# Performance work log

Measured on AMD Instinct MI355X. Metric: run time of the kernel, lower is better.

The kernel has to match this reference:

```python
import jax, jax.numpy as jnp
import numpy as np

SCALING_FACTOR = 1.0


def setup_inputs() -> dict:
    key = jax.random.key(0)
    k1, k2, k3 = jax.random.split(key, 3)
    B, N1, N2, DX, DZ, NT, NK = 4, 64, 64, 2, 128, 2048, 2
    x_grid = jax.random.uniform(k1, (B, N1, N2, DX), dtype=jnp.float32)
    z_grid = jax.random.normal(k2, (B, N1, N2, DZ), dtype=jnp.float32)
    xt = jax.random.uniform(k3, (B, NT, DX), dtype=jnp.float32)
    # Replicates torch init: logspace around log10(init_lengthscale), inverse-softplus
    init_ls = np.logspace(np.log10(0.1) - 0.5, np.log10(0.1) + 0.5, NK).astype(np.float32)
    init_ls = np.tile(init_ls[None, :], (DX, 1))  # (dim, num_kernels)
    lengthscale_param = jnp.asarray(np.log(np.expm1(init_ls)))
    return {"x_grid": x_grid, "z_grid": z_grid, "xt": xt, "lengthscale_param": lengthscale_param}


def reference(x_grid, z_grid, xt, lengthscale_param):
    B = x_grid.shape[0]
    xg = x_grid.reshape(B, -1, x_grid.shape[-1])   # (b, ng, dx)
    zg = z_grid.reshape(B, -1, z_grid.shape[-1])   # (b, ng, dz)
    ls = 1e-5 + jax.nn.softplus(lengthscale_param)  # (dx, nk)
    # EQ/RBF weights: (b, nt, ng, nk)
    diff = (xt[:, :, None, :, None] - xg[:, None, :, :, None]) / ls[None, None, None]
    weights = jnp.exp(-0.5 * jnp.sum(diff * diff, axis=3))
    # weighted smoothing: per-kernel matmul weights @ z_grid, then interleave as (dz nk)
    out = jnp.einsum('btgk,bgz->btzk', weights, zg) / SCALING_FACTOR  # (b, nt, dz, nk)
    return out.reshape(B, xt.shape[1], -1)  # (b, nt, dz*nk), nk fastest like 'b nt (dz nk)'
```

## Files before the change

### kernel.cpp

```cpp
#include <hip/hip_runtime.h>
#include <hip/hip_bf16.h>
#include <cmath>

#define B_   4
#define NT_  2048
#define G_   4096
#define DZ_  128

typedef __attribute__((ext_vector_type(8))) short bf16x8;
typedef __attribute__((ext_vector_type(8))) short s16x8;
typedef __attribute__((ext_vector_type(4))) float f32x4;

__device__ __forceinline__ float softplus_f(float x) {
    return fmaxf(x, 0.0f) + log1pf(expf(-fabsf(x)));
}

__device__ __forceinline__ void gl2lds16(const void* gsrc, void* ldst) {
    __builtin_amdgcn_global_load_lds(
        (const __attribute__((address_space(1))) unsigned int*)gsrc,
        (__attribute__((address_space(3))) unsigned int*)ldst, 16, 0, 0);
}

__global__ __launch_bounds__(256, 1)
void transpose_z(const float* __restrict__ z, unsigned short* __restrict__ zt)
{
    __shared__ unsigned short tile[64][66];
    const int bx = blockIdx.x;
    const int zti = bx & 1;
    const int gt  = (bx >> 1) & 63;
    const int b   = bx >> 7;
    const int g0 = gt * 64, z0 = zti * 64;
    const int tid = threadIdx.x;
    const int zl = tid & 63, gl = tid >> 6;
    #pragma unroll
    for (int i = 0; i < 16; ++i) {
        const int g = gl + i * 4;
        const float v = z[(size_t)(b * G_ + g0 + g) * DZ_ + z0 + zl];
        unsigned int u = __float_as_uint(v);
        u = u + 0x7FFFu + ((u >> 16) & 1u);
        tile[g][zl] = (unsigned short)(u >> 16);
    }
    __syncthreads();
    const int nt  = tid >> 6;
    const int q   = (tid >> 4) & 3;
    const int fl  = tid & 15;
    #pragma unroll
    for (int i = 0; i < 2; ++i) {
        s16x8 v;
        #pragma unroll
        for (int j = 0; j < 8; ++j)
            v[j] = (short)tile[i * 32 + q * 8 + j][nt * 16 + fl];
        *(s16x8*)(zt + ((size_t)(b * 128 + gt * 2 + i) * 8 + zti * 4 + nt) * 512
                  + (size_t)(q * 16 + fl) * 8) = v;
    }
}

__global__ __launch_bounds__(512, 4)
void setconv_main(const float* __restrict__ xt,
                  const float* __restrict__ xg,
                  const float* __restrict__ lsp,
                  const unsigned short* __restrict__ Zt,
                  float* __restrict__ out)
{
    __shared__ __align__(16) unsigned short lds[32768];

    const int bx = blockIdx.x;
    const int b  = (bx >> 1) & 3;
    const int tt = ((bx >> 3) << 1) | (bx & 1);
    const int tid  = threadIdx.x;
    const int w    = tid >> 6;
    const int lane = tid & 63;
    const int quad = lane >> 4;
    const int l15  = lane & 15;
    const int t0   = tt * 16;

    float c00, c01, c10, c11;
    {
        const float h = -0.72134752f;
        float ls;
        ls = 1e-5f + softplus_f(lsp[0]); c00 = h / (ls * ls);
        ls = 1e-5f + softplus_f(lsp[1]); c01 = h / (ls * ls);
        ls = 1e-5f + softplus_f(lsp[2]); c10 = h / (ls * ls);
        ls = 1e-5f + softplus_f(lsp[3]); c11 = h / (ls * ls);
    }

    const float xt0 = xt[(size_t)(b * NT_ + t0 + l15) * 2 + 0];
    const float xt1 = xt[(size_t)(b * NT_ + t0 + l15) * 2 + 1];

    f32x4 acc[2][8];
    #pragma unroll
    for (int k = 0; k < 2; ++k)
        #pragma unroll
        for (int n = 0; n < 8; ++n) acc[k][n] = (f32x4)0.0f;

    unsigned short* const mytile = lds + w * 4096;
    const float* xgq = xg + (size_t)(b * G_ + w * 512 + quad * 8) * 2;

    float4 xv0 = *(const float4*)(xgq + 0);
    float4 xv1 = *(const float4*)(xgq + 4);
    float4 xv2 = *(const float4*)(xgq + 8);
    float4 xv3 = *(const float4*)(xgq + 12);
    {
        const unsigned short* zs = Zt + (size_t)(b * 128 + w * 16) * 4096 + lane * 8;
        #pragma unroll
        for (int i = 0; i < 8; ++i)
            gl2lds16(zs + i * 512, mytile + i * 512);
    }

    #pragma unroll
    for (int ch = 0; ch < 16; ++ch) {
        float gx[8], gy[8];
        gx[0]=xv0.x; gy[0]=xv0.y; gx[1]=xv0.z; gy[1]=xv0.w;
        gx[2]=xv1.x; gy[2]=xv1.y; gx[3]=xv1.z; gy[3]=xv1.w;
        gx[4]=xv2.x; gy[4]=xv2.y; gx[5]=xv2.z; gy[5]=xv2.w;
        gx[6]=xv3.x; gy[6]=xv3.y; gx[7]=xv3.z; gy[7]=xv3.w;
        unsigned int w0b[8], w1b[8];
        #pragma unroll
        for (int j = 0; j < 8; ++j) {
            const float d0 = xt0 - gx[j];
            const float d1 = xt1 - gy[j];
            const float q0 = d0 * d0;
            const float q1 = d1 * d1;
            const float e0 = fmaf(q1, c10, q0 * c00);
            const float e1 = fmaf(q1, c11, q0 * c01);
            w0b[j] = __float_as_uint(__builtin_amdgcn_exp2f(e0));
            w1b[j] = __float_as_uint(__builtin_amdgcn_exp2f(e1));
        }
        union { bf16x8 v; unsigned int u[4]; } a0, a1;
        #pragma unroll
        for (int h = 0; h < 4; ++h) {
            a0.u[h] = __builtin_amdgcn_perm(w0b[2*h+1], w0b[2*h], 0x07060302u);
            a1.u[h] = __builtin_amdgcn_perm(w1b[2*h+1], w1b[2*h], 0x07060302u);
        }

        __builtin_amdgcn_s_waitcnt(0x0F70);
        if (ch < 15) {
            const float* xp = xgq + (ch + 1) * 64;
            xv0 = *(const float4*)(xp + 0);
            xv1 = *(const float4*)(xp + 4);
            xv2 = *(const float4*)(xp + 8);
            xv3 = *(const float4*)(xp + 12);
        }

        #pragma unroll
        for (int nt = 0; nt < 8; ++nt) {
            const bf16x8 bz = *(const bf16x8*)(mytile + nt * 512 + lane * 8);
            acc[0][nt] = __builtin_amdgcn_mfma_f32_16x16x32_bf16(a0.v, bz, acc[0][nt], 0, 0, 0);
            acc[1][nt] = __builtin_amdgcn_mfma_f32_16x16x32_bf16(a1.v, bz, acc[1][nt], 0, 0, 0);
        }

        if (ch < 15) {
            const unsigned short* zs = Zt + (size_t)(b * 128 + w * 16 + ch + 1) * 4096
                                       + lane * 8;
            #pragma unroll
            for (int i = 0; i < 8; ++i)
                gl2lds16(zs + i * 512, mytile + i * 512);
        }
    }

    float* const red = (float*)lds;
    #define RED_W(slot) { \
        float* bp = &red[(slot) * 4096 + lane * 4]; \
        _Pragma("unroll") \
        for (int k = 0; k < 2; ++k) \
            _Pragma("unroll") \
            for (int n = 0; n < 8; ++n) \
                *(f32x4*)(bp + (k * 8 + n) * 256) = acc[k][n]; }
    #define RED_A(slot) { \
        const float* bp = &red[(slot) * 4096 + lane * 4]; \
        _Pragma("unroll") \
        for (int k = 0; k < 2; ++k) \
            _Pragma("unroll") \
            for (int n = 0; n < 8; ++n) \
                acc[k][n] += *(const f32x4*)(bp + (k * 8 + n) * 256); }

    __syncthreads();
    if (w >= 4) RED_W(w - 4);
    __syncthreads();
    if (w < 4) RED_A(w);
    if (w == 2 || w == 3) RED_W(w);
    __syncthreads();
    if (w < 2) RED_A(w + 2);
    if (w == 1) RED_W(3);
    __syncthreads();
    if (w == 0) {
        RED_A(3);
        const int tr = t0 + quad * 4;
        #pragma unroll
        for (int nt = 0; nt < 8; ++nt) {
            float* ob = out + (size_t)(b * NT_ + tr) * (DZ_ * 2) + (nt * 16 + l15) * 2;
            #pragma unroll
            for (int r = 0; r < 4; ++r)
                *(float2*)(ob + (size_t)r * (DZ_ * 2)) =
                    make_float2(acc[0][nt][r], acc[1][nt][r]);
        }
    }
    #undef RED_W
    #undef RED_A
}

extern "C" void kernel_launch(void* const* d_in, const int* in_sizes, int n_in,
                              void* d_out, int out_size, void* d_ws, size_t ws_size,
                              hipStream_t stream)
{
    const float* x_grid = (const float*)d_in[0];
    const float* z_grid = (const float*)d_in[1];
    const float* xt     = (const float*)d_in[2];
    const float* lsp    = (const float*)d_in[3];
    float* out = (float*)d_out;
    unsigned short* Zt = (unsigned short*)d_ws;

    hipLaunchKernelGGL(transpose_z, dim3(512), dim3(256), 0, stream, z_grid, Zt);
    hipLaunchKernelGGL(setconv_main, dim3(512), dim3(512), 0, stream,
                       xt, x_grid, lsp, Zt, out);
}
```

Baseline: 101.7 us.

## Load Z tiles directly into registers instead of staging through LDS

```diff
diff --git a/kernel.cpp b/kernel.cpp
--- a/kernel.cpp
+++ b/kernel.cpp
@@ -13,12 +13,6 @@
 
 __device__ __forceinline__ float softplus_f(float x) {
     return fmaxf(x, 0.0f) + log1pf(expf(-fabsf(x)));
-}
-
-__device__ __forceinline__ void gl2lds16(const void* gsrc, void* ldst) {
-    __builtin_amdgcn_global_load_lds(
-        (const __attribute__((address_space(1))) unsigned int*)gsrc,
-        (__attribute__((address_space(3))) unsigned int*)ldst, 16, 0, 0);
 }
 
 __global__ __launch_bounds__(256, 1)
@@ -62,7 +56,7 @@
                   const unsigned short* __restrict__ Zt,
                   float* __restrict__ out)
 {
-    __shared__ __align__(16) unsigned short lds[32768];
+    __shared__ __align__(16) float red[16384];
 
     const int bx = blockIdx.x;
     const int b  = (bx >> 1) & 3;
@@ -93,72 +87,66 @@
         #pragma unroll
         for (int n = 0; n < 8; ++n) acc[k][n] = (f32x4)0.0f;
 
-    unsigned short* const mytile = lds + w * 4096;
+    const unsigned short* zb = Zt + (size_t)(b * 128 + w * 16) * 4096 + lane * 8;
     const float* xgq = xg + (size_t)(b * G_ + w * 512 + quad * 8) * 2;
 
     float4 xv0 = *(const float4*)(xgq + 0);
     float4 xv1 = *(const float4*)(xgq + 4);
     float4 xv2 = *(const float4*)(xgq + 8);
     float4 xv3 = *(const float4*)(xgq + 12);
-    {
-        const unsigned short* zs = Zt + (size_t)(b * 128 + w * 16) * 4096 + lane * 8;
-        #pragma unroll
-        for (int i = 0; i < 8; ++i)
-            gl2lds16(zs + i * 512, mytile + i * 512);
-    }
-
-    #pragma unroll
+    bf16x8 bz[8];
+    #pragma unroll
+    for (int nt = 0; nt < 8; ++nt)
+        bz[nt] = *(const bf16x8*)(zb + nt * 512);
+
+    #pragma unroll 1
     for (int ch = 0; ch < 16; ++ch) {
-        float gx[8], gy[8];
-        gx[0]=xv0.x; gy[0]=xv0.y; gx[1]=xv0.z; gy[1]=xv0.w;
-        gx[2]=xv1.x; gy[2]=xv1.y; gx[3]=xv1.z; gy[3]=xv1.w;
-        gx[4]=xv2.x; gy[4]=xv2.y; gx[5]=xv2.z; gy[5]=xv2.w;
-        gx[6]=xv3.x; gy[6]=xv3.y; gx[7]=xv3.z; gy[7]=xv3.w;
-        unsigned int w0b[8], w1b[8];
-        #pragma unroll
-        for (int j = 0; j < 8; ++j) {
-            const float d0 = xt0 - gx[j];
-            const float d1 = xt1 - gy[j];
-            const float q0 = d0 * d0;
-            const float q1 = d1 * d1;
-            const float e0 = fmaf(q1, c10, q0 * c00);
-            const float e1 = fmaf(q1, c11, q0 * c01);
-            w0b[j] = __float_as_uint(__builtin_amdgcn_exp2f(e0));
-            w1b[j] = __float_as_uint(__builtin_amdgcn_exp2f(e1));
-        }
         union { bf16x8 v; unsigned int u[4]; } a0, a1;
         #pragma unroll
-        for (int h = 0; h < 4; ++h) {
-            a0.u[h] = __builtin_amdgcn_perm(w0b[2*h+1], w0b[2*h], 0x07060302u);
-            a1.u[h] = __builtin_amdgcn_perm(w1b[2*h+1], w1b[2*h], 0x07060302u);
-        }
-
-        __builtin_amdgcn_s_waitcnt(0x0F70);
+        for (int jg = 0; jg < 2; ++jg) {
+            const float4 xa = jg ? xv2 : xv0;
+            const float4 xb = jg ? xv3 : xv1;
+            const float px[4] = {xa.x, xa.z, xb.x, xb.z};
+            const float py[4] = {xa.y, xa.w, xb.y, xb.w};
+            unsigned int w0b[4], w1b[4];
+            #pragma unroll
+            for (int j = 0; j < 4; ++j) {
+                const float d0 = xt0 - px[j];
+                const float d1 = xt1 - py[j];
+                const float q0 = d0 * d0;
+                const float q1 = d1 * d1;
+                const float e0 = fmaf(q1, c10, q0 * c00);
+                const float e1 = fmaf(q1, c11, q0 * c01);
+                w0b[j] = __float_as_uint(__builtin_amdgcn_exp2f(e0));
+                w1b[j] = __float_as_uint(__builtin_amdgcn_exp2f(e1));
+            }
+            a0.u[jg * 2 + 0] = __builtin_amdgcn_perm(w0b[1], w0b[0], 0x07060302u);
+            a0.u[jg * 2 + 1] = __builtin_amdgcn_perm(w0b[3], w0b[2], 0x07060302u);
+            a1.u[jg * 2 + 0] = __builtin_amdgcn_perm(w1b[1], w1b[0], 0x07060302u);
+            a1.u[jg * 2 + 1] = __builtin_amdgcn_perm(w1b[3], w1b[2], 0x07060302u);
+        }
+
+        __builtin_amdgcn_s_setprio(1);
+        #pragma unroll
+        for (int nt = 0; nt < 8; ++nt) {
+            acc[0][nt] = __builtin_amdgcn_mfma_f32_16x16x32_bf16(a0.v, bz[nt], acc[0][nt], 0, 0, 0);
+            acc[1][nt] = __builtin_amdgcn_mfma_f32_16x16x32_bf16(a1.v, bz[nt], acc[1][nt], 0, 0, 0);
+        }
+        __builtin_amdgcn_s_setprio(0);
+
         if (ch < 15) {
             const float* xp = xgq + (ch + 1) * 64;
             xv0 = *(const float4*)(xp + 0);
             xv1 = *(const float4*)(xp + 4);
             xv2 = *(const float4*)(xp + 8);
             xv3 = *(const float4*)(xp + 12);
-        }
-
-        #pragma unroll
-        for (int nt = 0; nt < 8; ++nt) {
-            const bf16x8 bz = *(const bf16x8*)(mytile + nt * 512 + lane * 8);
-            acc[0][nt] = __builtin_amdgcn_mfma_f32_16x16x32_bf16(a0.v, bz, acc[0][nt], 0, 0, 0);
-            acc[1][nt] = __builtin_amdgcn_mfma_f32_16x16x32_bf16(a1.v, bz, acc[1][nt], 0, 0, 0);
-        }
-
-        if (ch < 15) {
-            const unsigned short* zs = Zt + (size_t)(b * 128 + w * 16 + ch + 1) * 4096
-                                       + lane * 8;
+            const unsigned short* zc = zb + (size_t)(ch + 1) * 4096;
             #pragma unroll
-            for (int i = 0; i < 8; ++i)
-                gl2lds16(zs + i * 512, mytile + i * 512);
-        }
-    }
-
-    float* const red = (float*)lds;
+            for (int nt = 0; nt < 8; ++nt)
+                bz[nt] = *(const bf16x8*)(zc + nt * 512);
+        }
+    }
+
     #define RED_W(slot) { \
         float* bp = &red[(slot) * 4096 + lane * 4]; \
         _Pragma("unroll") \
```

New measurement: 123.5 us. 1.21x slower.
